# Optimization experiments

Hardware: AMD Instinct MI355X
Metric: run time of the kernel (lower is better)

Reference implementation:

```python
import jax, jax.numpy as jnp
import numpy as np

# Phi-2 prefill geometry
B, S = 4, 1024            # 4 packed sequences of length 1024 (cu_seqlen_prefill path)
T = B * S                 # total flat tokens
H = 32                    # num_attention_heads
D = 80                    # head_size = hidden // heads
HID = H * D               # 2560
ROT = 32                  # rotary_dim = partial_rotary_factor(0.4) * head_size
HALF = ROT // 2
ROPE_THETA = 10000.0
SOFTMAX_SCALE = D ** -0.5


def setup_inputs() -> dict:
    key = jax.random.key(0)
    k0, k1, k2, k3, k4 = jax.random.split(key, 5)
    hidden_states = jax.random.normal(k0, (T, HID), dtype=jnp.float32)
    # positions restart per sequence (equal-length packed prefill)
    pos = jnp.tile(jnp.arange(S, dtype=jnp.float32), B)              # [T]
    inv_freq = 1.0 / (ROPE_THETA ** (jnp.arange(0, ROT, 2, dtype=jnp.float32) / ROT))  # [HALF]
    freqs = pos[:, None] * inv_freq[None, :]                         # [T, HALF]
    cos = jnp.cos(freqs)
    sin = jnp.sin(freqs)
    w_qkv = jax.random.normal(k1, (HID + 2 * HID, HID), dtype=jnp.float32) * 0.02
    b_qkv = jax.random.normal(k2, (HID + 2 * HID,), dtype=jnp.float32) * 0.02
    w_dense = jax.random.normal(k3, (HID, HID), dtype=jnp.float32) * 0.02
    b_dense = jax.random.normal(k4, (HID,), dtype=jnp.float32) * 0.02
    return {"hidden_states": hidden_states, "cos": cos, "sin": sin,
            "w_qkv": w_qkv, "b_qkv": b_qkv, "w_dense": w_dense, "b_dense": b_dense}


def _apply_partial_rotary(x, cos, sin):
    # x: [T, h, D]; rotate first ROT dims, GPT-NeoX half-split style (as in
    # lorax PositionRotaryEmbedding); remaining D-ROT dims pass through.
    x1 = x[..., :HALF]
    x2 = x[..., HALF:ROT]
    x_pass = x[..., ROT:]
    c = cos[:, None, :]  # [T,1,HALF]
    s = sin[:, None, :]
    o1 = x1 * c - x2 * s
    o2 = x2 * c + x1 * s
    return jnp.concatenate([o1, o2, x_pass], axis=-1)


def reference(hidden_states, cos, sin, w_qkv, b_qkv, w_dense, b_dense):
    # fused QKV projection (torch Linear: x @ W.T + b)
    qkv = hidden_states @ w_qkv.T + b_qkv                  # [T, 3*HID]
    q = qkv[:, :HID].reshape(T, H, D)
    k = qkv[:, HID:2 * HID].reshape(T, H, D)
    v = qkv[:, 2 * HID:].reshape(T, H, D)
    # rotary applied to query and key (key = kv[:,0]) before cache write
    q = _apply_partial_rotary(q, cos, sin)
    k = _apply_partial_rotary(k, cos, sin)
    # flash_attn prefill == varlen causal attention; equal-length packing
    # lets us batch it as [B,S,H,D]
    qb = q.reshape(B, S, H, D)
    kb = k.reshape(B, S, H, D)
    vb = v.reshape(B, S, H, D)
    scores = jnp.einsum("bqhd,bkhd->bhqk", qb, kb) * SOFTMAX_SCALE  # [B,H,S,S]
    causal = jnp.tril(jnp.ones((S, S), dtype=bool))
    scores = jnp.where(causal[None, None], scores, jnp.finfo(scores.dtype).min)
    attn = jax.nn.softmax(scores, axis=-1)
    out = jnp.einsum("bhqk,bkhd->bqhd", attn, vb)          # [B,S,H,D]
    out = out.reshape(T, HID)
    return out @ w_dense.T + b_dense                        # [T, HID]
```

## Files before the change

kernel.cpp:

```cpp
#include <hip/hip_runtime.h>

typedef __attribute__((ext_vector_type(8))) __bf16 bf16x8;
typedef __attribute__((ext_vector_type(4))) float f32x4;

#define NH 32
#define DH 80
#define SEQ 1024
#define NB 4
#define NT 4096
#define HID 2560
#define NQKV 7680
#define SM_SCALE 0.11180339887498948f
#define QSCALE 0.16131381648337428f

static __device__ __forceinline__ unsigned short f2bf(float f) {
  unsigned u = __builtin_bit_cast(unsigned, f);
  u += 0x7fffu + ((u >> 16) & 1u);
  return (unsigned short)(u >> 16);
}
static __device__ __forceinline__ float bf2f(unsigned short s) {
  unsigned u = (unsigned)s << 16;
  return __builtin_bit_cast(float, u);
}

typedef __attribute__((address_space(1))) const unsigned int as1_uint;
typedef __attribute__((address_space(3))) unsigned int as3_uint;
static __device__ __forceinline__ void gload16(const void* g, void* l) {
  __builtin_amdgcn_global_load_lds((as1_uint*)g, (as3_uint*)l, 16, 0, 0);
}

__global__ __launch_bounds__(256) void cvt3_kernel(
    const float* __restrict__ s0, unsigned short* __restrict__ d0, int n0,
    const float* __restrict__ s1, unsigned short* __restrict__ d1, int n1,
    const float* __restrict__ s2, unsigned short* __restrict__ d2, int n2) {
  const int ntot = n0 + n1 + n2;
  for (int i = blockIdx.x * blockDim.x + threadIdx.x; i < ntot;
       i += gridDim.x * blockDim.x) {
    const float4* __restrict__ s;
    ushort4* __restrict__ d;
    int j;
    if (i < n0) {
      s = (const float4*)s0; d = (ushort4*)d0; j = i;
    } else if (i < n0 + n1) {
      s = (const float4*)s1; d = (ushort4*)d1; j = i - n0;
    } else {
      s = (const float4*)s2; d = (ushort4*)d2; j = i - n0 - n1;
    }
    float4 v = s[j];
    ushort4 o;
    o.x = f2bf(v.x);
    o.y = f2bf(v.y);
    o.z = f2bf(v.z);
    o.w = f2bf(v.w);
    d[j] = o;
  }
}

template <int EPI>
__global__ __launch_bounds__(512, 2) void gemm8p_kernel(
    const unsigned short* __restrict__ A, const unsigned short* __restrict__ Bm,
    const float* __restrict__ bias, unsigned short* __restrict__ Cq,
    unsigned short* __restrict__ Ck, unsigned short* __restrict__ Cv,
    float* __restrict__ Cf, int M, int N, int K) {
  __shared__ __align__(16) unsigned short AL[2][2][8192];
  __shared__ __align__(16) unsigned short BL[2][2][8192];
  const int tid = threadIdx.x;
  const int lane = tid & 63, w = tid >> 6;
  const int wm = w >> 2, wn = w & 3;
  const int lr = lane & 15, lg = lane >> 4;
  const int bhh = wn >> 1;
  const int brow = (wn & 1) * 64;

  const int gx = gridDim.x;
  const int nwg = gx * gridDim.y;
  int bid = blockIdx.y * gx + blockIdx.x;
  bid = (bid & 7) * (nwg >> 3) + (bid >> 3);
  const int n0 = (bid % gx) * 256;
  const int m0 = (bid / gx) * 256;

  const unsigned short* asrc[2][2];
  const unsigned short* bsrc[2][2];
#pragma unroll
  for (int h = 0; h < 2; ++h)
#pragma unroll
    for (int j = 0; j < 2; ++j) {
      const int off = j * 8192 + tid * 16;
      const int u = off ^ (((off >> 7) & 7) << 4);
      const int row = u >> 7, col = (u & 127) >> 1;
      asrc[h][j] = A + (size_t)(m0 + h * 128 + row) * K + col;
      bsrc[h][j] = Bm + (size_t)(n0 + h * 128 + row) * K + col;
    }

  const int NK = K >> 6, NIT = NK >> 1;

#define SA(buf, h, kt)                                                     \
  do {                                                                     \
    gload16(asrc[h][0] + (size_t)(kt) * 64,                                \
            (char*)&AL[buf][h][0] + w * 1024);                             \
    gload16(asrc[h][1] + (size_t)(kt) * 64,                                \
            (char*)&AL[buf][h][0] + 8192 + w * 1024);                      \
  } while (0)
#define SB(buf, h, kt)                                                     \
  do {                                                                     \
    gload16(bsrc[h][0] + (size_t)(kt) * 64,                                \
            (char*)&BL[buf][h][0] + w * 1024);                             \
    gload16(bsrc[h][1] + (size_t)(kt) * 64,                                \
            (char*)&BL[buf][h][0] + 8192 + w * 1024);                      \
  } while (0)
#define FA(buf, lrow, ks)                                                  \
  (*(const bf16x8*)((const char*)&AL[buf][wm][0] +                         \
                    (((lrow) * 128 + (ks) * 64 + lg * 16) ^                \
                     (((lrow) & 7) << 4))))
#define FB(buf, lrow, ks)                                                  \
  (*(const bf16x8*)((const char*)&BL[buf][bhh][0] +                        \
                    (((lrow) * 128 + (ks) * 64 + lg * 16) ^                \
                     (((lrow) & 7) << 4))))
#define PH_MFMA(AIDX, NBASE, BREG)                                         \
  __builtin_amdgcn_s_barrier();                                            \
  __builtin_amdgcn_s_setprio(1);                                           \
  _Pragma("unroll") for (int mf = 0; mf < 4; ++mf)                         \
      _Pragma("unroll") for (int nf = 0; nf < 2; ++nf) {                   \
    acc[AIDX + mf][NBASE + nf] = __builtin_amdgcn_mfma_f32_16x16x32_bf16(  \
        af[mf * 2 + 0], BREG[nf * 2 + 0], acc[AIDX + mf][NBASE + nf], 0, 0, 0); \
    acc[AIDX + mf][NBASE + nf] = __builtin_amdgcn_mfma_f32_16x16x32_bf16(  \
        af[mf * 2 + 1], BREG[nf * 2 + 1], acc[AIDX + mf][NBASE + nf], 0, 0, 0); \
  }                                                                        \
  __builtin_amdgcn_s_setprio(0);

  f32x4 acc[8][4];
#pragma unroll
  for (int i = 0; i < 8; ++i)
#pragma unroll
    for (int j = 0; j < 4; ++j) acc[i][j] = (f32x4)0.0f;

  SB(0, 0, 0); SB(0, 1, 0); SA(0, 0, 0); SA(0, 1, 0);
  SB(1, 0, 1); SB(1, 1, 1); SA(1, 0, 1); SA(1, 1, 1);
  asm volatile("s_waitcnt vmcnt(8)" ::: "memory");
  __builtin_amdgcn_s_barrier();

  bf16x8 af[8], bl[4], bhf[4];

  for (int i = 0; i < NIT; ++i) {
    const int t2 = 2 * i + 2, t3 = 2 * i + 3;
    const bool pf = (i + 1) < NIT;

#pragma unroll
    for (int mf = 0; mf < 4; ++mf) {
      af[mf * 2 + 0] = FA(0, mf * 16 + lr, 0);
      af[mf * 2 + 1] = FA(0, mf * 16 + lr, 1);
    }
#pragma unroll
    for (int nf = 0; nf < 2; ++nf) {
      bl[nf * 2 + 0] = FB(0, brow + nf * 16 + lr, 0);
      bl[nf * 2 + 1] = FB(0, brow + nf * 16 + lr, 1);
    }
    PH_MFMA(0, 0, bl)
    __builtin_amdgcn_s_barrier();
#pragma unroll
    for (int nf = 0; nf < 2; ++nf) {
      bhf[nf * 2 + 0] = FB(0, brow + (nf + 2) * 16 + lr, 0);
      bhf[nf * 2 + 1] = FB(0, brow + (nf + 2) * 16 + lr, 1);
    }
    PH_MFMA(0, 2, bhf)
    __builtin_amdgcn_s_barrier();
#pragma unroll
    for (int mf = 0; mf < 4; ++mf) {
      af[mf * 2 + 0] = FA(0, 64 + mf * 16 + lr, 0);
      af[mf * 2 + 1] = FA(0, 64 + mf * 16 + lr, 1);
    }
    if (pf) { SB(0, 0, t2); SB(0, 1, t2); }
    PH_MFMA(4, 0, bl)
    __builtin_amdgcn_s_barrier();
    if (pf) { SA(0, 0, t2); SA(0, 1, t2); }
    PH_MFMA(4, 2, bhf)
    if (pf)
      asm volatile("s_waitcnt vmcnt(8)" ::: "memory");
    else
      asm volatile("s_waitcnt vmcnt(0)" ::: "memory");
    __builtin_amdgcn_s_barrier();

#pragma unroll
    for (int mf = 0; mf < 4; ++mf) {
      af[mf * 2 + 0] = FA(1, mf * 16 + lr, 0);
      af[mf * 2 + 1] = FA(1, mf * 16 + lr, 1);
    }
#pragma unroll
    for (int nf = 0; nf < 2; ++nf) {
      bl[nf * 2 + 0] = FB(1, brow + nf * 16 + lr, 0);
      bl[nf * 2 + 1] = FB(1, brow + nf * 16 + lr, 1);
    }
    PH_MFMA(0, 0, bl)
    __builtin_amdgcn_s_barrier();
#pragma unroll
    for (int nf = 0; nf < 2; ++nf) {
      bhf[nf * 2 + 0] = FB(1, brow + (nf + 2) * 16 + lr, 0);
      bhf[nf * 2 + 1] = FB(1, brow + (nf + 2) * 16 + lr, 1);
    }
    PH_MFMA(0, 2, bhf)
    __builtin_amdgcn_s_barrier();
#pragma unroll
    for (int mf = 0; mf < 4; ++mf) {
      af[mf * 2 + 0] = FA(1, 64 + mf * 16 + lr, 0);
      af[mf * 2 + 1] = FA(1, 64 + mf * 16 + lr, 1);
    }
    if (pf) { SB(1, 0, t3); SB(1, 1, t3); }
    PH_MFMA(4, 0, bl)
    __builtin_amdgcn_s_barrier();
    if (pf) { SA(1, 0, t3); SA(1, 1, t3); }
    PH_MFMA(4, 2, bhf)
    if (pf) asm volatile("s_waitcnt vmcnt(8)" ::: "memory");
    __builtin_amdgcn_s_barrier();
  }
#undef SA
#undef SB
#undef FA
#undef FB
#undef PH_MFMA

  if (EPI == 0) {
    if (n0 >= 2 * HID) {
      unsigned short* scr = (unsigned short*)&AL[0][0][0] + w * 2176;
      const int bb = (m0 + wm * 128) >> 10;
      const int ssb = (m0 + wm * 128) & 1023;
#pragma unroll
      for (int nf = 0; nf < 4; ++nf) {
        const int col0 = n0 - 2 * HID + wn * 64 + nf * 16;
        const int hh = col0 / DH;
        const int dd0 = col0 - hh * DH;
        const float bv = bias[2 * HID + col0 + lr];
#pragma unroll
        for (int mf = 0; mf < 8; ++mf) {
          ushort4 p;
          p.x = f2bf(acc[mf][nf][0] + bv);
          p.y = f2bf(acc[mf][nf][1] + bv);
          p.z = f2bf(acc[mf][nf][2] + bv);
          p.w = f2bf(acc[mf][nf][3] + bv);
          *(ushort4*)&scr[lr * 136 + mf * 16 + lg * 4] = p;
        }
#pragma unroll
        for (int it = 0; it < 4; ++it) {
          const int dd = (lane >> 4) + it * 4;
          const int sl = (lane & 15) * 8;
          bf16x8 v = *(const bf16x8*)&scr[dd * 136 + sl];
          *(bf16x8*)(Cv + ((size_t)(bb * NH + hh) * DH + dd0 + dd) * SEQ + ssb + sl) = v;
        }
        asm volatile("s_waitcnt lgkmcnt(0)" ::: "memory");
      }
    } else {
#pragma unroll
      for (int nf = 0; nf < 4; ++nf) {
        const int col = n0 + wn * 64 + nf * 16 + lr;
        const int sec = col >= HID ? 1 : 0;
        const int rem = col - sec * HID;
        const int hh = rem / DH;
        const int dd = rem - hh * DH;
        unsigned short* dst = sec ? Ck : Cq;
        const float bv = bias[col];
#pragma unroll
        for (int mf = 0; mf < 8; ++mf) {
#pragma unroll
          for (int r = 0; r < 4; ++r) {
            const int tr = m0 + wm * 128 + mf * 16 + lg * 4 + r;
            const int bb2 = tr >> 10, ss = tr & 1023;
            dst[((size_t)(bb2 * NH + hh) * SEQ + ss) * DH + dd] =
                f2bf(acc[mf][nf][r] + bv);
          }
        }
      }
    }
  } else {
#pragma unroll
    for (int nf = 0; nf < 4; ++nf) {
      const int col = n0 + wn * 64 + nf * 16 + lr;
      const float bv = bias[col];
#pragma unroll
      for (int mf = 0; mf < 8; ++mf)
#pragma unroll
        for (int r = 0; r < 4; ++r) {
          const int row = m0 + wm * 128 + mf * 16 + lg * 4 + r;
          Cf[row * N + col] = acc[mf][nf][r] + bv;
        }
    }
  }
}

__global__ __launch_bounds__(512, 2) void gemmd8p_kernel(
    const unsigned short* __restrict__ A, const unsigned short* __restrict__ Bm,
    const float* __restrict__ bias, float* __restrict__ Cf, int M, int N, int K) {
  __shared__ __align__(16) unsigned short AL[2][8192];
  __shared__ __align__(16) unsigned short BL[2][20480];
  const int tid = threadIdx.x;
  const int lane = tid & 63, w = tid >> 6;
  const int wm = w >> 2, wn = w & 3;
  const int lr = lane & 15, lg = lane >> 4;

  const int gx = gridDim.x;
  const int nwg = gx * gridDim.y;
  int bid = blockIdx.y * gx + blockIdx.x;
  bid = (bid & 7) * (nwg >> 3) + (bid >> 3);
  const int n0 = (bid % gx) * 320;
  const int m0 = (bid / gx) * 128;

  const unsigned short* asrc[2];
  const unsigned short* bsrc[5];
#pragma unroll
  for (int j = 0; j < 2; ++j) {
    const int off = j * 8192 + tid * 16;
    const int u = off ^ (((off >> 7) & 7) << 4);
    const int row = u >> 7, col = (u & 127) >> 1;
    asrc[j] = A + (size_t)(m0 + row) * K + col;
  }
#pragma unroll
  for (int j = 0; j < 5; ++j) {
    const int off = j * 8192 + tid * 16;
    const int u = off ^ (((off >> 7) & 7) << 4);
    const int row = u >> 7, col = (u & 127) >> 1;
    bsrc[j] = Bm + (size_t)(n0 + row) * K + col;
  }

  const int NK = K >> 6;

#define DSTG(buf, kt)                                                       \
  do {                                                                      \
    gload16(asrc[0] + (size_t)(kt) * 64, (char*)&AL[buf][0] + tid * 16);    \
    gload16(asrc[1] + (size_t)(kt) * 64,                                    \
            (char*)&AL[buf][0] + 8192 + tid * 16);                          \
    gload16(bsrc[0] + (size_t)(kt) * 64, (char*)&BL[buf][0] + tid * 16);    \
    gload16(bsrc[1] + (size_t)(kt) * 64,                                    \
            (char*)&BL[buf][0] + 8192 + tid * 16);                          \
    gload16(bsrc[2] + (size_t)(kt) * 64,                                    \
            (char*)&BL[buf][0] + 16384 + tid * 16);                         \
    gload16(bsrc[3] + (size_t)(kt) * 64,                                    \
            (char*)&BL[buf][0] + 24576 + tid * 16);                         \
    gload16(bsrc[4] + (size_t)(kt) * 64,                                    \
            (char*)&BL[buf][0] + 32768 + tid * 16);                         \
  } while (0)
#define DFA(buf, lrow, ks)                                                  \
  (*(const bf16x8*)((const char*)&AL[buf][0] +                              \
                    (((lrow) * 128 + (ks) * 64 + lg * 16) ^                 \
                     (((lrow) & 7) << 4))))
#define DFB(buf, lrow, ks)                                                  \
  (*(const bf16x8*)((const char*)&BL[buf][0] +                              \
                    (((lrow) * 128 + (ks) * 64 + lg * 16) ^                 \
                     (((lrow) & 7) << 4))))

  f32x4 acc[4][5];
#pragma unroll
  for (int i = 0; i < 4; ++i)
#pragma unroll
    for (int j = 0; j < 5; ++j) acc[i][j] = (f32x4)0.0f;

  DSTG(0, 0);
  asm volatile("s_waitcnt vmcnt(0)" ::: "memory");
  __builtin_amdgcn_s_barrier();

  for (int t = 0; t < NK; ++t) {
    const int buf = t & 1, nb = buf ^ 1;
    const bool pf = (t + 1) < NK;
    bf16x8 afr[4], bfr[5];

#pragma unroll
    for (int mf = 0; mf < 4; ++mf) afr[mf] = DFA(buf, wm * 64 + mf * 16 + lr, 0);
#pragma unroll
    for (int nf = 0; nf < 5; ++nf) bfr[nf] = DFB(buf, wn * 80 + nf * 16 + lr, 0);
    if (pf) DSTG(nb, t + 1);
    __builtin_amdgcn_s_barrier();
    __builtin_amdgcn_s_setprio(1);
#pragma unroll
    for (int mf = 0; mf < 4; ++mf)
#pragma unroll
      for (int nf = 0; nf < 5; ++nf)
        acc[mf][nf] = __builtin_amdgcn_mfma_f32_16x16x32_bf16(afr[mf], bfr[nf],
                                                              acc[mf][nf], 0, 0, 0);
    __builtin_amdgcn_s_setprio(0);
    __builtin_amdgcn_s_barrier();

#pragma unroll
    for (int mf = 0; mf < 4; ++mf) afr[mf] = DFA(buf, wm * 64 + mf * 16 + lr, 1);
#pragma unroll
    for (int nf = 0; nf < 5; ++nf) bfr[nf] = DFB(buf, wn * 80 + nf * 16 + lr, 1);
    __builtin_amdgcn_s_barrier();
    __builtin_amdgcn_s_setprio(1);
#pragma unroll
    for (int mf = 0; mf < 4; ++mf)
#pragma unroll
      for (int nf = 0; nf < 5; ++nf)
        acc[mf][nf] = __builtin_amdgcn_mfma_f32_16x16x32_bf16(afr[mf], bfr[nf],
                                                              acc[mf][nf], 0, 0, 0);
    __builtin_amdgcn_s_setprio(0);
    if (pf) asm volatile("s_waitcnt vmcnt(0)" ::: "memory");
    __builtin_amdgcn_s_barrier();
  }
#undef DSTG
#undef DFA
#undef DFB

#pragma unroll
  for (int nf = 0; nf < 5; ++nf) {
    const int col = n0 + wn * 80 + nf * 16 + lr;
    const float bv = bias[col];
#pragma unroll
    for (int mf = 0; mf < 4; ++mf)
#pragma unroll
      for (int r = 0; r < 4; ++r) {
        const int row = m0 + wm * 64 + mf * 16 + lg * 4 + r;
        Cf[(size_t)row * N + col] = acc[mf][nf][r] + bv;
      }
  }
}

__global__ __launch_bounds__(256) void rope_kernel(unsigned short* __restrict__ Q,
                                                   unsigned short* __restrict__ K,
                                                   const float* __restrict__ cosb,
                                                   const float* __restrict__ sinb) {
  const int idx = blockIdx.x * 256 + threadIdx.x;
  const int i = idx & 15;
  const int s = (idx >> 4) & 1023;
  const int bh = idx >> 14;
  const int b = bh >> 5;
  const int t = b * SEQ + s;
  const float c = cosb[t * 16 + i];
  const float sn = sinb[t * 16 + i];
  const int base = (bh * SEQ + s) * DH;
  float q1 = bf2f(Q[base + i]), q2 = bf2f(Q[base + 16 + i]);
  Q[base + i] = f2bf((q1 * c - q2 * sn) * QSCALE);
  Q[base + 16 + i] = f2bf((q2 * c + q1 * sn) * QSCALE);
#pragma unroll
  for (int j = 0; j < 3; ++j) {
    const int d = 32 + j * 16 + i;
    Q[base + d] = f2bf(bf2f(Q[base + d]) * QSCALE);
  }
  float k1 = bf2f(K[base + i]), k2 = bf2f(K[base + 16 + i]);
  K[base + i] = f2bf(k1 * c - k2 * sn);
  K[base + 16 + i] = f2bf(k2 * c + k1 * sn);
}

__global__ __launch_bounds__(512) void attn_kernel(const unsigned short* __restrict__ Qb,
                                                   const unsigned short* __restrict__ Kb,
                                                   const unsigned short* __restrict__ Vg,
                                                   unsigned short* __restrict__ Ob) {
  __shared__ __align__(16) unsigned short Klds[64][104];
  __shared__ __align__(16) unsigned short Vt[80][72];
  __shared__ __align__(16) unsigned short Plds[8][32][72];
  const int tid = threadIdx.x;
  const int lane = tid & 63, w = tid >> 6;
  const int lr = lane & 15, lg = lane >> 4;
  const int koff = lg * 8;
  const int bh = blockIdx.y;
  const int h = bh & 31;
  const int base = bh * (SEQ * DH);
  const int vbase = bh * (DH * SEQ);

  for (int e = tid; e < 64 * 16; e += 512) Klds[e >> 4][80 + (e & 15)] = 0;

  const int ke0r = tid / 10, ke0c = (tid - (tid / 10) * 10) * 8;
  const int ke1 = tid + 512;
  const int ke1r = ke1 / 10, ke1c = (ke1 - (ke1 / 10) * 10) * 8;
  const int ve0d = tid >> 3, ve0c = (tid & 7) * 8;
  const int ve1d = (tid + 512) >> 3, ve1c = ((tid + 512) & 7) * 8;

  const int qts[2] = {(int)blockIdx.x, 3 - (int)blockIdx.x};

  for (int sub = 0; sub < 2; ++sub) {
    const int qt = qts[sub];
    const int rowbase = qt * 256 + w * 32;

    bf16x8 qf[2][3];
#pragma unroll
    for (int hh = 0; hh < 2; ++hh)
#pragma unroll
      for (int c = 0; c < 3; ++c) {
        const int d = c * 32 + koff;
        if (d < DH)
          qf[hh][c] =
              *(const bf16x8*)(Qb + base + (rowbase + hh * 16 + lr) * DH + d);
        else
          qf[hh][c] = (bf16x8)(__bf16)0.0f;
      }

    float m[2][4], l[2][4];
    f32x4 of[2][5];
#pragma unroll
    for (int hh = 0; hh < 2; ++hh) {
#pragma unroll
      for (int r = 0; r < 4; ++r) {
        m[hh][r] = -3.0e38f;
        l[hh][r] = 0.0f;
      }
#pragma unroll
      for (int d = 0; d < 5; ++d) of[hh][d] = (f32x4)0.0f;
    }

    bf16x8 kreg0, kreg1, vreg0, vreg1;
    kreg0 = *(const bf16x8*)(Kb + base + ke0r * DH + ke0c);
    if (tid < 128) kreg1 = *(const bf16x8*)(Kb + base + ke1r * DH + ke1c);
    vreg0 = *(const bf16x8*)(Vg + vbase + ve0d * SEQ + ve0c);
    if (tid < 128) vreg1 = *(const bf16x8*)(Vg + vbase + ve1d * SEQ + ve1c);

    const int ktmax = 4 * qt + 3;
    for (int kt = 0; kt <= ktmax; ++kt) {
      __syncthreads();
      *(bf16x8*)&Klds[ke0r][ke0c] = kreg0;
      if (tid < 128) *(bf16x8*)&Klds[ke1r][ke1c] = kreg1;
      *(bf16x8*)&Vt[ve0d][ve0c] = vreg0;
      if (tid < 128) *(bf16x8*)&Vt[ve1d][ve1c] = vreg1;
      __syncthreads();

      if (kt < ktmax) {
        const int nb = (kt + 1) * 64;
        kreg0 = *(const bf16x8*)(Kb + base + (nb + ke0r) * DH + ke0c);
        if (tid < 128) kreg1 = *(const bf16x8*)(Kb + base + (nb + ke1r) * DH + ke1c);
        vreg0 = *(const bf16x8*)(Vg + vbase + ve0d * SEQ + nb + ve0c);
        if (tid < 128) vreg1 = *(const bf16x8*)(Vg + vbase + ve1d * SEQ + nb + ve1c);
      }

      if (kt * 64 > rowbase + 31) continue;
      const bool fullvis = (kt * 64 + 63 <= rowbase);

      f32x4 sc[2][4];
#pragma unroll
      for (int hh = 0; hh < 2; ++hh)
#pragma unroll
        for (int cf = 0; cf < 4; ++cf) sc[hh][cf] = (f32x4)0.0f;
#pragma unroll
      for (int c = 0; c < 3; ++c) {
#pragma unroll
        for (int cf = 0; cf < 4; ++cf) {
          bf16x8 kb = *(const bf16x8*)&Klds[cf * 16 + lr][c * 32 + koff];
          sc[0][cf] = __builtin_amdgcn_mfma_f32_16x16x32_bf16(qf[0][c], kb, sc[0][cf], 0, 0, 0);
          sc[1][cf] = __builtin_amdgcn_mfma_f32_16x16x32_bf16(qf[1][c], kb, sc[1][cf], 0, 0, 0);
        }
      }

#pragma unroll
      for (int hh = 0; hh < 2; ++hh) {
        if (!fullvis) {
          const int rowg = rowbase + hh * 16 + lg * 4;
#pragma unroll
          for (int cf = 0; cf < 4; ++cf) {
            const int colg = kt * 64 + cf * 16 + lr;
#pragma unroll
            for (int r = 0; r < 4; ++r)
              if (colg > rowg + r) sc[hh][cf][r] = -1.0e30f;
          }
        }
        float mx[4];
#pragma unroll
        for (int r = 0; r < 4; ++r) {
          float v = fmaxf(fmaxf(sc[hh][0][r], sc[hh][1][r]),
                          fmaxf(sc[hh][2][r], sc[hh][3][r]));
#pragma unroll
          for (int off = 1; off < 16; off <<= 1) v = fmaxf(v, __shfl_xor(v, off, 64));
          mx[r] = v;
        }
        bool need = false;
#pragma unroll
        for (int r = 0; r < 4; ++r) need |= (mx[r] > m[hh][r] + 11.54f);
        if (__ballot(need)) {
          float al[4];
#pragma unroll
          for (int r = 0; r < 4; ++r) {
            const float mn = fmaxf(m[hh][r], mx[r]);
            al[r] = exp2f(m[hh][r] - mn);
            m[hh][r] = mn;
          }
#pragma unroll
          for (int d = 0; d < 5; ++d)
#pragma unroll
            for (int r = 0; r < 4; ++r) of[hh][d][r] *= al[r];
#pragma unroll
          for (int r = 0; r < 4; ++r) l[hh][r] *= al[r];
        }
        float ls[4] = {0.f, 0.f, 0.f, 0.f};
#pragma unroll
        for (int cf = 0; cf < 4; ++cf)
#pragma unroll
          for (int r = 0; r < 4; ++r) {
            const float p = exp2f(sc[hh][cf][r] - m[hh][r]);
            sc[hh][cf][r] = p;
            ls[r] += p;
          }
#pragma unroll
        for (int r = 0; r < 4; ++r) {
          float sv = ls[r];
#pragma unroll
          for (int off = 1; off < 16; off <<= 1) sv += __shfl_xor(sv, off, 64);
          l[hh][r] += sv;
        }
#pragma unroll
        for (int cf = 0; cf < 4; ++cf)
#pragma unroll
          for (int r = 0; r < 4; ++r)
            Plds[w][hh * 16 + lg * 4 + r][cf * 16 + lr] = f2bf(sc[hh][cf][r]);
      }

#pragma unroll
      for (int kc = 0; kc < 2; ++kc) {
        bf16x8 pa0 = *(const bf16x8*)&Plds[w][lr][kc * 32 + koff];
        bf16x8 pa1 = *(const bf16x8*)&Plds[w][16 + lr][kc * 32 + koff];
#pragma unroll
        for (int d = 0; d < 5; ++d) {
          bf16x8 vb = *(const bf16x8*)&Vt[d * 16 + lr][kc * 32 + koff];
          of[0][d] = __builtin_amdgcn_mfma_f32_16x16x32_bf16(pa0, vb, of[0][d], 0, 0, 0);
          of[1][d] = __builtin_amdgcn_mfma_f32_16x16x32_bf16(pa1, vb, of[1][d], 0, 0, 0);
        }
      }
    }

#pragma unroll
    for (int hh = 0; hh < 2; ++hh) {
      const int t = (bh >> 5) * SEQ + rowbase + hh * 16 + lg * 4;
#pragma unroll
      for (int r = 0; r < 4; ++r) {
        const float rl = 1.0f / l[hh][r];
#pragma unroll
        for (int d = 0; d < 5; ++d)
          Ob[(t + r) * HID + h * DH + d * 16 + lr] = f2bf(of[hh][d][r] * rl);
      }
    }
  }
}

extern "C" void kernel_launch(void* const* d_in, const int* in_sizes, int n_in,
                              void* d_out, int out_size, void* d_ws, size_t ws_size,
                              hipStream_t stream) {
  const float* hs = (const float*)d_in[0];
  const float* cosb = (const float*)d_in[1];
  const float* sinb = (const float*)d_in[2];
  const float* w_qkv = (const float*)d_in[3];
  const float* b_qkv = (const float*)d_in[4];
  const float* w_dense = (const float*)d_in[5];
  const float* b_dense = (const float*)d_in[6];
  float* out = (float*)d_out;
  char* ws = (char*)d_ws;

  unsigned short* hsb = (unsigned short*)(ws + 0);
  unsigned short* aob = (unsigned short*)(ws + 0);
  unsigned short* wqb = (unsigned short*)(ws + 20971520);
  unsigned short* wdb = (unsigned short*)(ws + 20971520);
  unsigned short* wdb2 = (unsigned short*)(ws + 123207680);
  unsigned short* Qb = (unsigned short*)(ws + 60293120);
  unsigned short* Kb = (unsigned short*)(ws + 81264640);
  unsigned short* Vb = (unsigned short*)(ws + 102236160);
  (void)wdb;

  cvt3_kernel<<<2048, 256, 0, stream>>>(hs, hsb, (NT * HID) / 4,
                                        w_qkv, wqb, (NQKV * HID) / 4,
                                        w_dense, wdb2, (HID * HID) / 4);
  gemm8p_kernel<0><<<dim3(NQKV / 256, NT / 256), 512, 0, stream>>>(
      hsb, wqb, b_qkv, Qb, Kb, Vb, nullptr, NT, NQKV, HID);
  rope_kernel<<<(NB * NH * SEQ * 16) / 256, 256, 0, stream>>>(Qb, Kb, cosb, sinb);
  attn_kernel<<<dim3(2, NB * NH), 512, 0, stream>>>(Qb, Kb, Vb, aob);
  gemmd8p_kernel<<<dim3(HID / 320, NT / 128), 512, 0, stream>>>(
      aob, wdb2, b_dense, out, NT, HID, HID);
}
```

Baseline: 347.6 us.

## Restructure GEMM main loops to fewer barriers per k-tile

Rewrites the QKV GEMM main loop from a manually unrolled two-tile, eight-phase schedule into a per-k-tile loop. It loads both halves of the B fragments up front and issues the MFMAs in two larger phases with only two barriers per tile. The dense-projection GEMM likewise loads both k-halves of its fragments at once and runs a single MFMA phase per tile, removing two barriers. This cuts synchronisation overhead but uses more fragment registers and gives less fine-grained interleaving of loads with MFMAs, which could hurt latency hiding.

```diff
diff --git a/kernel.cpp b/kernel.cpp
--- a/kernel.cpp
+++ b/kernel.cpp
@@ -91,7 +91,7 @@
       bsrc[h][j] = Bm + (size_t)(n0 + h * 128 + row) * K + col;
     }
 
-  const int NK = K >> 6, NIT = NK >> 1;
+  const int NK = K >> 6;
 
 #define SA(buf, h, kt)                                                     \
   do {                                                                     \
@@ -115,17 +115,6 @@
   (*(const bf16x8*)((const char*)&BL[buf][bhh][0] +                        \
                     (((lrow) * 128 + (ks) * 64 + lg * 16) ^                \
                      (((lrow) & 7) << 4))))
-#define PH_MFMA(AIDX, NBASE, BREG)                                         \
-  __builtin_amdgcn_s_barrier();                                            \
-  __builtin_amdgcn_s_setprio(1);                                           \
-  _Pragma("unroll") for (int mf = 0; mf < 4; ++mf)                         \
-      _Pragma("unroll") for (int nf = 0; nf < 2; ++nf) {                   \
-    acc[AIDX + mf][NBASE + nf] = __builtin_amdgcn_mfma_f32_16x16x32_bf16(  \
-        af[mf * 2 + 0], BREG[nf * 2 + 0], acc[AIDX + mf][NBASE + nf], 0, 0, 0); \
-    acc[AIDX + mf][NBASE + nf] = __builtin_amdgcn_mfma_f32_16x16x32_bf16(  \
-        af[mf * 2 + 1], BREG[nf * 2 + 1], acc[AIDX + mf][NBASE + nf], 0, 0, 0); \
-  }                                                                        \
-  __builtin_amdgcn_s_setprio(0);
 
   f32x4 acc[8][4];
 #pragma unroll
@@ -138,84 +127,77 @@
   asm volatile("s_waitcnt vmcnt(8)" ::: "memory");
   __builtin_amdgcn_s_barrier();
 
-  bf16x8 af[8], bl[4], bhf[4];
-
-  for (int i = 0; i < NIT; ++i) {
-    const int t2 = 2 * i + 2, t3 = 2 * i + 3;
-    const bool pf = (i + 1) < NIT;
+  for (int t = 0; t < NK; ++t) {
+    const int buf = t & 1;
+    const int tn = t + 2;
+    const bool pf = tn < NK;
+    bf16x8 af[8], blr[4], bhr[4];
 
 #pragma unroll
     for (int mf = 0; mf < 4; ++mf) {
-      af[mf * 2 + 0] = FA(0, mf * 16 + lr, 0);
-      af[mf * 2 + 1] = FA(0, mf * 16 + lr, 1);
+      af[mf * 2 + 0] = FA(buf, mf * 16 + lr, 0);
+      af[mf * 2 + 1] = FA(buf, mf * 16 + lr, 1);
     }
 #pragma unroll
     for (int nf = 0; nf < 2; ++nf) {
-      bl[nf * 2 + 0] = FB(0, brow + nf * 16 + lr, 0);
-      bl[nf * 2 + 1] = FB(0, brow + nf * 16 + lr, 1);
-    }
-    PH_MFMA(0, 0, bl)
+      blr[nf * 2 + 0] = FB(buf, brow + nf * 16 + lr, 0);
+      blr[nf * 2 + 1] = FB(buf, brow + nf * 16 + lr, 1);
+      bhr[nf * 2 + 0] = FB(buf, brow + (nf + 2) * 16 + lr, 0);
+      bhr[nf * 2 + 1] = FB(buf, brow + (nf + 2) * 16 + lr, 1);
+    }
+    __builtin_amdgcn_s_setprio(1);
+#pragma unroll
+    for (int mf = 0; mf < 4; ++mf)
+#pragma unroll
+      for (int nf = 0; nf < 2; ++nf) {
+        acc[mf][nf] = __builtin_amdgcn_mfma_f32_16x16x32_bf16(
+            af[mf * 2 + 0], blr[nf * 2 + 0], acc[mf][nf], 0, 0, 0);
+        acc[mf][nf] = __builtin_amdgcn_mfma_f32_16x16x32_bf16(
+            af[mf * 2 + 1], blr[nf * 2 + 1], acc[mf][nf], 0, 0, 0);
+        acc[mf][nf + 2] = __builtin_amdgcn_mfma_f32_16x16x32_bf16(
+            af[mf * 2 + 0], bhr[nf * 2 + 0], acc[mf][nf + 2], 0, 0, 0);
+        acc[mf][nf + 2] = __builtin_amdgcn_mfma_f32_16x16x32_bf16(
+            af[mf * 2 + 1], bhr[nf * 2 + 1], acc[mf][nf + 2], 0, 0, 0);
+      }
+    __builtin_amdgcn_s_setprio(0);
+    asm volatile("s_waitcnt lgkmcnt(0)" ::: "memory");
     __builtin_amdgcn_s_barrier();
-#pragma unroll
-    for (int nf = 0; nf < 2; ++nf) {
-      bhf[nf * 2 + 0] = FB(0, brow + (nf + 2) * 16 + lr, 0);
-      bhf[nf * 2 + 1] = FB(0, brow + (nf + 2) * 16 + lr, 1);
-    }
-    PH_MFMA(0, 2, bhf)
+    if (pf) { SB(buf, 0, tn); SB(buf, 1, tn); }
+
+#pragma unroll
+    for (int mf = 0; mf < 4; ++mf) {
+      af[mf * 2 + 0] = FA(buf, 64 + mf * 16 + lr, 0);
+      af[mf * 2 + 1] = FA(buf, 64 + mf * 16 + lr, 1);
+    }
+    __builtin_amdgcn_s_setprio(1);
+#pragma unroll
+    for (int mf = 0; mf < 4; ++mf)
+#pragma unroll
+      for (int nf = 0; nf < 2; ++nf) {
+        acc[mf + 4][nf] = __builtin_amdgcn_mfma_f32_16x16x32_bf16(
+            af[mf * 2 + 0], blr[nf * 2 + 0], acc[mf + 4][nf], 0, 0, 0);
+        acc[mf + 4][nf] = __builtin_amdgcn_mfma_f32_16x16x32_bf16(
+            af[mf * 2 + 1], blr[nf * 2 + 1], acc[mf + 4][nf], 0, 0, 0);
+        acc[mf + 4][nf + 2] = __builtin_amdgcn_mfma_f32_16x16x32_bf16(
+            af[mf * 2 + 0], bhr[nf * 2 + 0], acc[mf + 4][nf + 2], 0, 0, 0);
+        acc[mf + 4][nf + 2] = __builtin_amdgcn_mfma_f32_16x16x32_bf16(
+            af[mf * 2 + 1], bhr[nf * 2 + 1], acc[mf + 4][nf + 2], 0, 0, 0);
+      }
+    __builtin_amdgcn_s_setprio(0);
+    asm volatile("s_waitcnt lgkmcnt(0)" ::: "memory");
     __builtin_amdgcn_s_barrier();
-#pragma unroll
-    for (int mf = 0; mf < 4; ++mf) {
-      af[mf * 2 + 0] = FA(0, 64 + mf * 16 + lr, 0);
-      af[mf * 2 + 1] = FA(0, 64 + mf * 16 + lr, 1);
-    }
-    if (pf) { SB(0, 0, t2); SB(0, 1, t2); }
-    PH_MFMA(4, 0, bl)
-    __builtin_amdgcn_s_barrier();
-    if (pf) { SA(0, 0, t2); SA(0, 1, t2); }
-    PH_MFMA(4, 2, bhf)
+    if (pf) { SA(buf, 0, tn); SA(buf, 1, tn); }
+
     if (pf)
       asm volatile("s_waitcnt vmcnt(8)" ::: "memory");
-    else
+    else if (t + 1 < NK)
       asm volatile("s_waitcnt vmcnt(0)" ::: "memory");
-    __builtin_amdgcn_s_barrier();
-
-#pragma unroll
-    for (int mf = 0; mf < 4; ++mf) {
-      af[mf * 2 + 0] = FA(1, mf * 16 + lr, 0);
-      af[mf * 2 + 1] = FA(1, mf * 16 + lr, 1);
-    }
-#pragma unroll
-    for (int nf = 0; nf < 2; ++nf) {
-      bl[nf * 2 + 0] = FB(1, brow + nf * 16 + lr, 0);
-      bl[nf * 2 + 1] = FB(1, brow + nf * 16 + lr, 1);
-    }
-    PH_MFMA(0, 0, bl)
-    __builtin_amdgcn_s_barrier();
-#pragma unroll
-    for (int nf = 0; nf < 2; ++nf) {
-      bhf[nf * 2 + 0] = FB(1, brow + (nf + 2) * 16 + lr, 0);
-      bhf[nf * 2 + 1] = FB(1, brow + (nf + 2) * 16 + lr, 1);
-    }
-    PH_MFMA(0, 2, bhf)
-    __builtin_amdgcn_s_barrier();
-#pragma unroll
-    for (int mf = 0; mf < 4; ++mf) {
-      af[mf * 2 + 0] = FA(1, 64 + mf * 16 + lr, 0);
-      af[mf * 2 + 1] = FA(1, 64 + mf * 16 + lr, 1);
-    }
-    if (pf) { SB(1, 0, t3); SB(1, 1, t3); }
-    PH_MFMA(4, 0, bl)
-    __builtin_amdgcn_s_barrier();
-    if (pf) { SA(1, 0, t3); SA(1, 1, t3); }
-    PH_MFMA(4, 2, bhf)
-    if (pf) asm volatile("s_waitcnt vmcnt(8)" ::: "memory");
     __builtin_amdgcn_s_barrier();
   }
 #undef SA
 #undef SB
 #undef FA
 #undef FB
-#undef PH_MFMA
 
   if (EPI == 0) {
     if (n0 >= 2 * HID) {
@@ -357,37 +339,31 @@
   for (int t = 0; t < NK; ++t) {
     const int buf = t & 1, nb = buf ^ 1;
     const bool pf = (t + 1) < NK;
-    bf16x8 afr[4], bfr[5];
-
-#pragma unroll
-    for (int mf = 0; mf < 4; ++mf) afr[mf] = DFA(buf, wm * 64 + mf * 16 + lr, 0);
-#pragma unroll
-    for (int nf = 0; nf < 5; ++nf) bfr[nf] = DFB(buf, wn * 80 + nf * 16 + lr, 0);
     if (pf) DSTG(nb, t + 1);
-    __builtin_amdgcn_s_barrier();
+
+    bf16x8 afr[8], bfr[10];
+#pragma unroll
+    for (int mf = 0; mf < 4; ++mf) {
+      afr[mf * 2 + 0] = DFA(buf, wm * 64 + mf * 16 + lr, 0);
+      afr[mf * 2 + 1] = DFA(buf, wm * 64 + mf * 16 + lr, 1);
+    }
+#pragma unroll
+    for (int nf = 0; nf < 5; ++nf) {
+      bfr[nf * 2 + 0] = DFB(buf, wn * 80 + nf * 16 + lr, 0);
+      bfr[nf * 2 + 1] = DFB(buf, wn * 80 + nf * 16 + lr, 1);
+    }
     __builtin_amdgcn_s_setprio(1);
 #pragma unroll
     for (int mf = 0; mf < 4; ++mf)
 #pragma unroll
-      for (int nf = 0; nf < 5; ++nf)
-        acc[mf][nf] = __builtin_amdgcn_mfma_f32_16x16x32_bf16(afr[mf], bfr[nf],
-                                                              acc[mf][nf], 0, 0, 0);
+      for (int nf = 0; nf < 5; ++nf) {
+        acc[mf][nf] = __builtin_amdgcn_mfma_f32_16x16x32_bf16(
+            afr[mf * 2 + 0], bfr[nf * 2 + 0], acc[mf][nf], 0, 0, 0);
+        acc[mf][nf] = __builtin_amdgcn_mfma_f32_16x16x32_bf16(
+            afr[mf * 2 + 1], bfr[nf * 2 + 1], acc[mf][nf], 0, 0, 0);
+      }
     __builtin_amdgcn_s_setprio(0);
-    __builtin_amdgcn_s_barrier();
-
-#pragma unroll
-    for (int mf = 0; mf < 4; ++mf) afr[mf] = DFA(buf, wm * 64 + mf * 16 + lr, 1);
-#pragma unroll
-    for (int nf = 0; nf < 5; ++nf) bfr[nf] = DFB(buf, wn * 80 + nf * 16 + lr, 1);
-    __builtin_amdgcn_s_barrier();
-    __builtin_amdgcn_s_setprio(1);
-#pragma unroll
-    for (int mf = 0; mf < 4; ++mf)
-#pragma unroll
-      for (int nf = 0; nf < 5; ++nf)
-        acc[mf][nf] = __builtin_amdgcn_mfma_f32_16x16x32_bf16(afr[mf], bfr[nf],
-                                                              acc[mf][nf], 0, 0, 0);
-    __builtin_amdgcn_s_setprio(0);
+    asm volatile("s_waitcnt lgkmcnt(0)" ::: "memory");
     if (pf) asm volatile("s_waitcnt vmcnt(0)" ::: "memory");
     __builtin_amdgcn_s_barrier();
   }
@@ -637,12 +613,10 @@
   unsigned short* hsb = (unsigned short*)(ws + 0);
   unsigned short* aob = (unsigned short*)(ws + 0);
   unsigned short* wqb = (unsigned short*)(ws + 20971520);
-  unsigned short* wdb = (unsigned short*)(ws + 20971520);
   unsigned short* wdb2 = (unsigned short*)(ws + 123207680);
   unsigned short* Qb = (unsigned short*)(ws + 60293120);
   unsigned short* Kb = (unsigned short*)(ws + 81264640);
   unsigned short* Vb = (unsigned short*)(ws + 102236160);
-  (void)wdb;
 
   cvt3_kernel<<<2048, 256, 0, stream>>>(hs, hsb, (NT * HID) / 4,
                                         w_qkv, wqb, (NQKV * HID) / 4,
```

After: 373.3 us. +7.4%, slower.
